# Performance work log

Hardware: AMD Instinct MI355X
Metric: run time of the kernel (lower is better)

## Reference

```python
import jax, jax.numpy as jnp
import numpy as np
import math

SCALE = 64.0
MARGIN = 0.5
THRESH = math.cos(math.pi - MARGIN)          # cos(pi - m)
MM = math.sin(math.pi - MARGIN) * MARGIN     # sin(pi - m) * m
N, D, C = 512, 512, 100000


def setup_inputs() -> dict:
    key = jax.random.key(0)
    k1, k2, k3 = jax.random.split(key, 3)
    x = jax.random.normal(k1, (N, D), dtype=jnp.float32)
    label = jax.random.randint(k2, (N,), 0, C, dtype=jnp.int64)
    # reset_parameters: uniform(-stdv, stdv), stdv = 1/sqrt(in_features)
    stdv = 1.0 / math.sqrt(D)
    weight = jax.random.uniform(k3, (C, D), dtype=jnp.float32, minval=-stdv, maxval=stdv)
    return {"input": x, "label": label, "weight": weight}


def reference(input, label, weight):
    # row-wise L2 normalize features and class weights
    ex = input / jnp.linalg.norm(input, axis=1, keepdims=True)
    ew = weight / jnp.linalg.norm(weight, axis=1, keepdims=True)
    cos = jnp.einsum("nd,cd->nc", ex, ew)               # [N, C]
    rows = jnp.arange(cos.shape[0])
    cos_l = cos[rows, label]                              # cos at the label column
    cond = cos_l > THRESH                                 # easy-margin condition per row
    onehot = (jnp.arange(cos.shape[1])[None, :] == label[:, None])
    a = jnp.where(onehot & cond[:, None], MARGIN, 0.0).astype(cos.dtype)
    b = jnp.where(onehot & (~cond[:, None]), -MM, 0.0).astype(cos.dtype)
    # clamp slightly inside [-1,1] to guard acos against fp roundoff
    cos_c = jnp.clip(cos, -1.0 + 1e-7, 1.0 - 1e-7)
    logits = SCALE * (jnp.cos(jnp.arccos(cos_c) + a) + b)
    return logits
```

## Files before the change

### kernel.cpp

```cpp
#include <hip/hip_runtime.h>
#include <hip/hip_bf16.h>
#include <stdint.h>


#define NROWS 512
#define DDIM 512
#define NCLS 100000

typedef __attribute__((ext_vector_type(8))) short bf16x8;
typedef __attribute__((ext_vector_type(8))) unsigned short u16x8;
typedef __attribute__((ext_vector_type(4))) float f32x4;

__device__ __forceinline__ unsigned short f2bf(float x) {
    union { float f; uint32_t u; } c; c.f = x;
    uint32_t r = (c.u + 0x7FFFu + ((c.u >> 16) & 1u)) >> 16;
    return (unsigned short)r;
}

__device__ __forceinline__ void g2lds16(const void* g, void* l) {
    __builtin_amdgcn_global_load_lds(
        (const __attribute__((address_space(1))) void*)g,
        (__attribute__((address_space(3))) void*)l, 16, 0, 0);
}

__global__ __launch_bounds__(256)
void rownorm_x(const float* __restrict__ in, unsigned short* __restrict__ out) {
    const int row  = blockIdx.x * 4 + (threadIdx.x >> 6);
    const int lane = threadIdx.x & 63;

    const float4* p = (const float4*)(in + (size_t)row * DDIM);
    float4 v0 = p[lane];
    float4 v1 = p[64 + lane];

    float ss = v0.x*v0.x + v0.y*v0.y + v0.z*v0.z + v0.w*v0.w
             + v1.x*v1.x + v1.y*v1.y + v1.z*v1.z + v1.w*v1.w;
    #pragma unroll
    for (int off = 32; off > 0; off >>= 1) ss += __shfl_xor(ss, off);
    const float r = rsqrtf(ss);

    unsigned short* orow = out + (size_t)row * DDIM;
    ushort4 o0, o1;
    o0.x = f2bf(v0.x * r); o0.y = f2bf(v0.y * r);
    o0.z = f2bf(v0.z * r); o0.w = f2bf(v0.w * r);
    o1.x = f2bf(v1.x * r); o1.y = f2bf(v1.y * r);
    o1.z = f2bf(v1.z * r); o1.w = f2bf(v1.w * r);
    *(ushort4*)(orow + lane * 4) = o0;
    *(ushort4*)(orow + 256 + lane * 4) = o1;
}

__global__ __launch_bounds__(256)
void arcface_gemm_fused(const unsigned short* __restrict__ A,
                        const float* __restrict__ W,
                        const int* __restrict__ labels,
                        float* __restrict__ out) {
    __shared__ unsigned short As[2][128 * 32];
    __shared__ unsigned short Bs[2][128 * 40];
    __shared__ float ssp[128];
    __shared__ int   lab_s[128];

    const int bid = blockIdx.x;
    int panel, slot;
    if (bid < 3104) { panel = (bid >> 5) * 8 + (bid & 7); slot = (bid >> 3) & 3; }
    else            { int l = bid - 3104; panel = 776 + l % 6; slot = l / 6; }
    const int rowBase = slot * 128;
    const int colBase = panel * 128;

    const int t    = threadIdx.x;
    const int lane = t & 63;
    const int wid  = t >> 6;
    const int wr   = wid >> 1;
    const int wc   = wid & 1;
    const int kg   = (lane >> 4) << 3;
    const int fr   = lane & 15;

    if (t < 128) lab_s[t] = labels[rowBase + t];

    const int brow = t >> 1;
    const int kc   = (t & 1) << 4;
    const int cls  = colBase + brow;
    const bool bv  = cls < NCLS;
    const float* gB = W + (size_t)(bv ? cls : 0) * DDIM + kc;
    unsigned short* wB[2] = { &Bs[0][brow * 40 + kc], &Bs[1][brow * 40 + kc] };

    const unsigned short* gA = A + (size_t)(rowBase + (t >> 2)) * DDIM + ((t & 3) << 3);

    float ss = 0.f;
    f32x4 acc[4][4] = {};

    float4 p0, p1, p2, p3;
    g2lds16(gA,             &As[0][t * 8]);
    g2lds16(gA + 64 * DDIM, &As[0][2048 + t * 8]);
    if (bv) {
        p0 = *(const float4*)(gB + 0);  p1 = *(const float4*)(gB + 4);
        p2 = *(const float4*)(gB + 8);  p3 = *(const float4*)(gB + 12);
    } else {
        p0 = float4{0,0,0,0}; p1 = p0; p2 = p0; p3 = p0;
    }

    #pragma unroll
    for (int tt = 0; tt < 16; ++tt) {
        const int cur = tt & 1;

        __builtin_amdgcn_s_barrier();
        __builtin_amdgcn_sched_barrier(0);
        asm volatile("s_waitcnt vmcnt(0)" ::: "memory");
        __builtin_amdgcn_sched_barrier(0);

        ss += p0.x*p0.x + p0.y*p0.y + p0.z*p0.z + p0.w*p0.w;
        ss += p1.x*p1.x + p1.y*p1.y + p1.z*p1.z + p1.w*p1.w;
        ss += p2.x*p2.x + p2.y*p2.y + p2.z*p2.z + p2.w*p2.w;
        ss += p3.x*p3.x + p3.y*p3.y + p3.z*p3.z + p3.w*p3.w;
        u16x8 o0, o1;
        o0[0]=f2bf(p0.x); o0[1]=f2bf(p0.y); o0[2]=f2bf(p0.z); o0[3]=f2bf(p0.w);
        o0[4]=f2bf(p1.x); o0[5]=f2bf(p1.y); o0[6]=f2bf(p1.z); o0[7]=f2bf(p1.w);
        o1[0]=f2bf(p2.x); o1[1]=f2bf(p2.y); o1[2]=f2bf(p2.z); o1[3]=f2bf(p2.w);
        o1[4]=f2bf(p3.x); o1[5]=f2bf(p3.y); o1[6]=f2bf(p3.z); o1[7]=f2bf(p3.w);
        *(u16x8*)(wB[cur])     = o0;
        *(u16x8*)(wB[cur] + 8) = o1;

        if (tt < 15) {
            const int kt = (tt + 1) * 32;
            g2lds16(gA + kt,             &As[cur ^ 1][t * 8]);
            g2lds16(gA + kt + 64 * DDIM, &As[cur ^ 1][2048 + t * 8]);
            if (bv) {
                p0 = *(const float4*)(gB + kt + 0);
                p1 = *(const float4*)(gB + kt + 4);
                p2 = *(const float4*)(gB + kt + 8);
                p3 = *(const float4*)(gB + kt + 12);
            }
        }

        asm volatile("s_waitcnt lgkmcnt(0)" ::: "memory");
        __builtin_amdgcn_sched_barrier(0);
        __builtin_amdgcn_s_barrier();
        __builtin_amdgcn_sched_barrier(0);

        bf16x8 a[4], b[4];
        #pragma unroll
        for (int m = 0; m < 4; ++m)
            a[m] = *(const bf16x8*)&As[cur][(wr * 64 + m * 16 + fr) * 32 + kg];
        #pragma unroll
        for (int n = 0; n < 4; ++n)
            b[n] = *(const bf16x8*)&Bs[cur][(wc * 64 + n * 16 + fr) * 40 + kg];

        #pragma unroll
        for (int m = 0; m < 4; ++m)
            #pragma unroll
            for (int n = 0; n < 4; ++n)
                acc[m][n] = __builtin_amdgcn_mfma_f32_16x16x32_bf16(
                    a[m], b[n], acc[m][n], 0, 0, 0);
    }

    float sst = ss + __shfl_xor(ss, 1);
    if ((t & 1) == 0) ssp[t >> 1] = sst;
    __syncthreads();

    const float lo = -1.0f + 1e-7f, hi = 1.0f - 1e-7f;
    const float COSM = 0.8775825618903728f;
    const float SINM = 0.479425538604203f;
    const float MM   = 0.2397127693021015f;
    const float THR  = -0.8775825618903728f;

    float rn[4];
    #pragma unroll
    for (int n = 0; n < 4; ++n)
        rn[n] = rsqrtf(ssp[wc * 64 + n * 16 + fr]);

    #pragma unroll
    for (int m = 0; m < 4; ++m) {
        const int rloc = wr * 64 + m * 16 + ((lane >> 4) << 2);
        #pragma unroll
        for (int n = 0; n < 4; ++n) {
            const int c = colBase + wc * 64 + n * 16 + fr;
            if (c < NCLS) {
                #pragma unroll
                for (int i = 0; i < 4; ++i) {
                    const float raw = acc[m][n][i] * rn[n];
                    const float tc  = fminf(fmaxf(raw, lo), hi);
                    float val = tc;
                    if (lab_s[rloc + i] == c) {
                        val = (raw > THR)
                            ? tc * COSM - sqrtf(fmaxf(1.0f - tc * tc, 0.0f)) * SINM
                            : tc - MM;
                    }
                    out[(size_t)(rowBase + rloc + i) * NCLS + c] = 64.0f * val;
                }
            }
        }
    }
}

extern "C" void kernel_launch(void* const* d_in, const int* in_sizes, int n_in,
                              void* d_out, int out_size, void* d_ws, size_t ws_size,
                              hipStream_t stream) {
    const float* x     = (const float*)d_in[0];
    const int*   label = (const int*)d_in[1];
    const float* w     = (const float*)d_in[2];
    float* out = (float*)d_out;

    unsigned short* Abf = (unsigned short*)d_ws;

    rownorm_x<<<NROWS / 4, 256, 0, stream>>>(x, Abf);

    arcface_gemm_fused<<<3128, 256, 0, stream>>>(Abf, w, label, out);
}
```

Measured before the change: 455.6 us.

## Drop LDS staging and feed MFMA operands directly from global memory

The GEMM kernel no longer stages A and B tiles through shared memory with barriers. Each wave loads its MFMA fragments straight from global memory (A from the bf16 workspace, W as fp32 converted with packed bf16 conversion instructions) and computes weight-row norms with lane shuffles. The column tile shrinks from 128 to 64, doubling the block count, and labels are read from global memory in the epilogue. This removes barrier and LDS overhead and raises parallelism, at the cost of redundant global/L2 reads of A and W across waves and less reuse per block.

```diff
diff --git a/kernel.cpp b/kernel.cpp
--- a/kernel.cpp
+++ b/kernel.cpp
@@ -4,11 +4,12 @@
 
 
 #define NROWS 512
-#define DDIM 512
-#define NCLS 100000
+#define DDIM  512
+#define NCLS  100000
+#define NCOLP 1563
+#define FULLP 1560
 
 typedef __attribute__((ext_vector_type(8))) short bf16x8;
-typedef __attribute__((ext_vector_type(8))) unsigned short u16x8;
 typedef __attribute__((ext_vector_type(4))) float f32x4;
 
 __device__ __forceinline__ unsigned short f2bf(float x) {
@@ -17,10 +18,10 @@
     return (unsigned short)r;
 }
 
-__device__ __forceinline__ void g2lds16(const void* g, void* l) {
-    __builtin_amdgcn_global_load_lds(
-        (const __attribute__((address_space(1))) void*)g,
-        (__attribute__((address_space(3))) void*)l, 16, 0, 0);
+__device__ __forceinline__ uint32_t cvtpk(float a, float b) {
+    uint32_t r;
+    asm("v_cvt_pk_bf16_f32 %0, %1, %2" : "=v"(r) : "v"(a), "v"(b));
+    return r;
 }
 
 __global__ __launch_bounds__(256)
@@ -49,111 +50,97 @@
 }
 
 __global__ __launch_bounds__(256)
-void arcface_gemm_fused(const unsigned short* __restrict__ A,
-                        const float* __restrict__ W,
-                        const int* __restrict__ labels,
-                        float* __restrict__ out) {
-    __shared__ unsigned short As[2][128 * 32];
-    __shared__ unsigned short Bs[2][128 * 40];
-    __shared__ float ssp[128];
-    __shared__ int   lab_s[128];
-
+void arcface_stream(const unsigned short* __restrict__ A,
+                    const float* __restrict__ W,
+                    const int* __restrict__ labels,
+                    float* __restrict__ out) {
     const int bid = blockIdx.x;
     int panel, slot;
-    if (bid < 3104) { panel = (bid >> 5) * 8 + (bid & 7); slot = (bid >> 3) & 3; }
-    else            { int l = bid - 3104; panel = 776 + l % 6; slot = l / 6; }
+    if (bid < FULLP * 4) { panel = (bid >> 5) * 8 + (bid & 7); slot = (bid >> 3) & 3; }
+    else                 { int l = bid - FULLP * 4; panel = FULLP + l % 3; slot = l / 3; }
     const int rowBase = slot * 128;
-    const int colBase = panel * 128;
+    const int colBase = panel * 64;
 
     const int t    = threadIdx.x;
     const int lane = t & 63;
     const int wid  = t >> 6;
     const int wr   = wid >> 1;
     const int wc   = wid & 1;
+    const int fr   = lane & 15;
     const int kg   = (lane >> 4) << 3;
-    const int fr   = lane & 15;
 
-    if (t < 128) lab_s[t] = labels[rowBase + t];
+    const unsigned short* aBase[4];
+    #pragma unroll
+    for (int m = 0; m < 4; ++m)
+        aBase[m] = A + (size_t)(rowBase + wr * 64 + m * 16 + fr) * DDIM + kg;
 
-    const int brow = t >> 1;
-    const int kc   = (t & 1) << 4;
-    const int cls  = colBase + brow;
-    const bool bv  = cls < NCLS;
-    const float* gB = W + (size_t)(bv ? cls : 0) * DDIM + kc;
-    unsigned short* wB[2] = { &Bs[0][brow * 40 + kc], &Bs[1][brow * 40 + kc] };
+    const float* bBase[2];
+    int bcls[2];
+    #pragma unroll
+    for (int n = 0; n < 2; ++n) {
+        bcls[n] = colBase + wc * 32 + n * 16 + fr;
+        const int cr = bcls[n] < NCLS ? bcls[n] : NCLS - 1;
+        bBase[n] = W + (size_t)cr * DDIM + kg;
+    }
 
-    const unsigned short* gA = A + (size_t)(rowBase + (t >> 2)) * DDIM + ((t & 3) << 3);
+    f32x4 acc[4][2] = {};
+    float ssq[2] = {0.f, 0.f};
 
-    float ss = 0.f;
-    f32x4 acc[4][4] = {};
-
-    float4 p0, p1, p2, p3;
-    g2lds16(gA,             &As[0][t * 8]);
-    g2lds16(gA + 64 * DDIM, &As[0][2048 + t * 8]);
-    if (bv) {
-        p0 = *(const float4*)(gB + 0);  p1 = *(const float4*)(gB + 4);
-        p2 = *(const float4*)(gB + 8);  p3 = *(const float4*)(gB + 12);
-    } else {
-        p0 = float4{0,0,0,0}; p1 = p0; p2 = p0; p3 = p0;
+    float4 fB[2][2];
+    #pragma unroll
+    for (int n = 0; n < 2; ++n) {
+        fB[n][0] = *(const float4*)(bBase[n] + 0);
+        fB[n][1] = *(const float4*)(bBase[n] + 4);
     }
 
     #pragma unroll
     for (int tt = 0; tt < 16; ++tt) {
-        const int cur = tt & 1;
+        const int kt = tt * 32;
 
-        __builtin_amdgcn_s_barrier();
-        __builtin_amdgcn_sched_barrier(0);
-        asm volatile("s_waitcnt vmcnt(0)" ::: "memory");
-        __builtin_amdgcn_sched_barrier(0);
+        bf16x8 a[4];
+        #pragma unroll
+        for (int m = 0; m < 4; ++m)
+            a[m] = *(const bf16x8*)(aBase[m] + kt);
 
-        ss += p0.x*p0.x + p0.y*p0.y + p0.z*p0.z + p0.w*p0.w;
-        ss += p1.x*p1.x + p1.y*p1.y + p1.z*p1.z + p1.w*p1.w;
-        ss += p2.x*p2.x + p2.y*p2.y + p2.z*p2.z + p2.w*p2.w;
-        ss += p3.x*p3.x + p3.y*p3.y + p3.z*p3.z + p3.w*p3.w;
-        u16x8 o0, o1;
-        o0[0]=f2bf(p0.x); o0[1]=f2bf(p0.y); o0[2]=f2bf(p0.z); o0[3]=f2bf(p0.w);
-        o0[4]=f2bf(p1.x); o0[5]=f2bf(p1.y); o0[6]=f2bf(p1.z); o0[7]=f2bf(p1.w);
-        o1[0]=f2bf(p2.x); o1[1]=f2bf(p2.y); o1[2]=f2bf(p2.z); o1[3]=f2bf(p2.w);
-        o1[4]=f2bf(p3.x); o1[5]=f2bf(p3.y); o1[6]=f2bf(p3.z); o1[7]=f2bf(p3.w);
-        *(u16x8*)(wB[cur])     = o0;
-        *(u16x8*)(wB[cur] + 8) = o1;
+        bf16x8 b[2];
+        #pragma unroll
+        for (int n = 0; n < 2; ++n) {
+            const float4 lo = fB[n][0], hi = fB[n][1];
+            ssq[n] += lo.x*lo.x + lo.y*lo.y + lo.z*lo.z + lo.w*lo.w
+                    + hi.x*hi.x + hi.y*hi.y + hi.z*hi.z + hi.w*hi.w;
+            uint32_t u0 = cvtpk(lo.x, lo.y);
+            uint32_t u1 = cvtpk(lo.z, lo.w);
+            uint32_t u2 = cvtpk(hi.x, hi.y);
+            uint32_t u3 = cvtpk(hi.z, hi.w);
+            union { uint32_t u[4]; bf16x8 v; } pk;
+            pk.u[0] = u0; pk.u[1] = u1; pk.u[2] = u2; pk.u[3] = u3;
+            b[n] = pk.v;
+        }
 
         if (tt < 15) {
-            const int kt = (tt + 1) * 32;
-            g2lds16(gA + kt,             &As[cur ^ 1][t * 8]);
-            g2lds16(gA + kt + 64 * DDIM, &As[cur ^ 1][2048 + t * 8]);
-            if (bv) {
-                p0 = *(const float4*)(gB + kt + 0);
-                p1 = *(const float4*)(gB + kt + 4);
-                p2 = *(const float4*)(gB + kt + 8);
-                p3 = *(const float4*)(gB + kt + 12);
+            #pragma unroll
+            for (int n = 0; n < 2; ++n) {
+                fB[n][0] = *(const float4*)(bBase[n] + kt + 32);
+                fB[n][1] = *(const float4*)(bBase[n] + kt + 36);
             }
         }
-
-        asm volatile("s_waitcnt lgkmcnt(0)" ::: "memory");
-        __builtin_amdgcn_sched_barrier(0);
-        __builtin_amdgcn_s_barrier();
-        __builtin_amdgcn_sched_barrier(0);
-
-        bf16x8 a[4], b[4];
-        #pragma unroll
-        for (int m = 0; m < 4; ++m)
-            a[m] = *(const bf16x8*)&As[cur][(wr * 64 + m * 16 + fr) * 32 + kg];
-        #pragma unroll
-        for (int n = 0; n < 4; ++n)
-            b[n] = *(const bf16x8*)&Bs[cur][(wc * 64 + n * 16 + fr) * 40 + kg];
 
         #pragma unroll
         for (int m = 0; m < 4; ++m)
             #pragma unroll
-            for (int n = 0; n < 4; ++n)
+            for (int n = 0; n < 2; ++n)
                 acc[m][n] = __builtin_amdgcn_mfma_f32_16x16x32_bf16(
                     a[m], b[n], acc[m][n], 0, 0, 0);
     }
 
-    float sst = ss + __shfl_xor(ss, 1);
-    if ((t & 1) == 0) ssp[t >> 1] = sst;
-    __syncthreads();
+    float rn[2];
+    #pragma unroll
+    for (int n = 0; n < 2; ++n) {
+        float s = ssq[n];
+        s += __shfl_xor(s, 16);
+        s += __shfl_xor(s, 32);
+        rn[n] = rsqrtf(s);
+    }
 
     const float lo = -1.0f + 1e-7f, hi = 1.0f - 1e-7f;
     const float COSM = 0.8775825618903728f;
@@ -161,29 +148,25 @@
     const float MM   = 0.2397127693021015f;
     const float THR  = -0.8775825618903728f;
 
-    float rn[4];
-    #pragma unroll
-    for (int n = 0; n < 4; ++n)
-        rn[n] = rsqrtf(ssp[wc * 64 + n * 16 + fr]);
-
     #pragma unroll
     for (int m = 0; m < 4; ++m) {
-        const int rloc = wr * 64 + m * 16 + ((lane >> 4) << 2);
         #pragma unroll
-        for (int n = 0; n < 4; ++n) {
-            const int c = colBase + wc * 64 + n * 16 + fr;
-            if (c < NCLS) {
-                #pragma unroll
-                for (int i = 0; i < 4; ++i) {
+        for (int i = 0; i < 4; ++i) {
+            const int r = rowBase + wr * 64 + m * 16 + ((lane >> 4) << 2) + i;
+            const int lab = labels[r];
+            #pragma unroll
+            for (int n = 0; n < 2; ++n) {
+                const int c = bcls[n];
+                if (c < NCLS) {
                     const float raw = acc[m][n][i] * rn[n];
                     const float tc  = fminf(fmaxf(raw, lo), hi);
                     float val = tc;
-                    if (lab_s[rloc + i] == c) {
+                    if (lab == c) {
                         val = (raw > THR)
                             ? tc * COSM - sqrtf(fmaxf(1.0f - tc * tc, 0.0f)) * SINM
                             : tc - MM;
                     }
-                    out[(size_t)(rowBase + rloc + i) * NCLS + c] = 64.0f * val;
+                    out[(size_t)r * NCLS + c] = 64.0f * val;
                 }
             }
         }
@@ -202,5 +185,5 @@
 
     rownorm_x<<<NROWS / 4, 256, 0, stream>>>(x, Abf);
 
-    arcface_gemm_fused<<<3128, 256, 0, stream>>>(Abf, w, label, out);
+    arcface_stream<<<NCOLP * 4, 256, 0, stream>>>(Abf, w, label, out);
 }
```

Measured after the change: 642.0 us. 1.41x slower.
